# Kernel tuning notes

Hardware: AMD Instinct MI355X
Metric: run time of the kernel (lower is better)

## Reference

```python
import jax, jax.numpy as jnp
import numpy as np
import math

B, C, L = 16, 512, 1024
CONV_NUM, NUM_HEAD, K = 4, 8, 7
LN_EPS = 1e-5


def layer_norm(h, g, b):
    # h: [..., C], normalize over last dim (matches nn.LayerNorm(hidden_size))
    mean = jnp.mean(h, axis=-1, keepdims=True)
    var = jnp.mean(jnp.square(h - mean), axis=-1, keepdims=True)
    return (h - mean) / jnp.sqrt(var + LN_EPS) * g + b


def timing_signal(length, channels):
    nt = channels // 2
    pos = jnp.arange(length, dtype=jnp.float32)
    log_inc = math.log(10000.0) / (nt - 1)
    inv = jnp.exp(jnp.arange(nt, dtype=jnp.float32) * -log_inc)
    st = pos[:, None] * inv[None, :]
    sig = jnp.concatenate([jnp.sin(st), jnp.cos(st)], axis=1)  # [L, 2*nt]
    if channels % 2:
        sig = jnp.pad(sig, ((0, 0), (0, 1)))
    return sig  # [L, C]


def setup_inputs() -> dict:
    key = jax.random.key(0)
    ks = jax.random.split(key, 20)
    s = 0.02
    inp = {
        'x': jax.random.normal(ks[0], (B, C, L), jnp.float32),
        'mask': jax.random.randint(ks[1], (B, L), 0, 2, jnp.int32),
        'layer': 1,
        'num_blks': 7,
        'dw_w': jax.random.normal(ks[2], (CONV_NUM, C, 1, K), jnp.float32) * s,
        'pw_w': jax.random.normal(ks[3], (CONV_NUM, C, C), jnp.float32) * s,
        'pw_b': jnp.zeros((CONV_NUM, C), jnp.float32),
        'conv_ln_g': jnp.ones((CONV_NUM, C), jnp.float32),
        'conv_ln_b': jnp.zeros((CONV_NUM, C), jnp.float32),
        'w_kv': jax.random.normal(ks[4], (2 * C, C), jnp.float32) * s,
        'b_kv': jnp.zeros((2 * C,), jnp.float32),
        'w_q': jax.random.normal(ks[5], (C, C), jnp.float32) * s,
        'b_q': jnp.zeros((C,), jnp.float32),
        'ln_att_g': jnp.ones((C,), jnp.float32),
        'ln_att_b': jnp.zeros((C,), jnp.float32),
        'w_ffd1': jax.random.normal(ks[6], (C, C), jnp.float32) * s,
        'b_ffd1': jnp.zeros((C,), jnp.float32),
        'w_ffd2': jax.random.normal(ks[7], (C, C), jnp.float32) * s,
        'b_ffd2': jnp.zeros((C,), jnp.float32),
        'ln_ffd_g': jnp.ones((C,), jnp.float32),
        'ln_ffd_b': jnp.zeros((C,), jnp.float32),
    }
    return inp


def _forward(x, maskf, dw_w, pw_w, pw_b, conv_ln_g, conv_ln_b, w_kv, b_kv, w_q,
             b_q, ln_att_g, ln_att_b, w_ffd1, b_ffd1, w_ffd2, b_ffd2,
             ln_ffd_g, ln_ffd_b):
    # eval mode: dropout is identity and layer_dropout (stochastic depth) is
    # skipped entirely (the residual add only happens when self.training).
    b, c, l = x.shape
    out = x + timing_signal(l, c).T[None]  # [B,C,L]

    for i in range(CONV_NUM):
        h = layer_norm(out.transpose(0, 2, 1), conv_ln_g[i], conv_ln_b[i])
        h = h.transpose(0, 2, 1)  # [B,C,L]
        # depthwise conv, groups=C, padding=k//2, no bias
        h = jax.lax.conv_general_dilated(
            h, dw_w[i], window_strides=(1,), padding=[(K // 2, K // 2)],
            feature_group_count=c, dimension_numbers=('NCH', 'OIH', 'NCH'))
        # pointwise 1x1 conv + relu
        h = jnp.einsum('oc,bcl->bol', pw_w[i], h) + pw_b[i][None, :, None]
        out = jax.nn.relu(h)

    # self-attention sublayer
    h = layer_norm(out.transpose(0, 2, 1), ln_att_g, ln_att_b)  # [B,L,C]
    kv = jnp.einsum('oc,blc->blo', w_kv, h) + b_kv  # [B,L,2C]
    q = jnp.einsum('oc,blc->blo', w_q, h) + b_q     # [B,L,C]
    dh = c // NUM_HEAD
    Kh = kv[..., :c].reshape(b, l, NUM_HEAD, dh).transpose(0, 2, 1, 3)
    Vh = kv[..., c:].reshape(b, l, NUM_HEAD, dh).transpose(0, 2, 1, 3)
    Qh = q.reshape(b, l, NUM_HEAD, dh).transpose(0, 2, 1, 3) * (dh ** -0.5)
    logits = jnp.einsum('bhqd,bhkd->bhqk', Qh, Kh)  # [B,H,L,L]
    m = maskf[:, None, None, :]
    logits = logits * m + (1.0 - m) * -1e30
    w = jax.nn.softmax(logits, axis=-1)
    att = jnp.einsum('bhqk,bhkd->bhqd', w, Vh)
    out = att.transpose(0, 2, 1, 3).reshape(b, l, c).transpose(0, 2, 1)  # [B,C,L]

    # feed-forward sublayer (two 1x1 convs)
    h = layer_norm(out.transpose(0, 2, 1), ln_ffd_g, ln_ffd_b).transpose(0, 2, 1)
    h = jax.nn.relu(jnp.einsum('oc,bcl->bol', w_ffd1, h) + b_ffd1[None, :, None])
    out = jnp.einsum('oc,bcl->bol', w_ffd2, h) + b_ffd2[None, :, None]
    return out


def reference(x, mask, layer, num_blks, dw_w, pw_w, pw_b, conv_ln_g, conv_ln_b,
              w_kv, b_kv, w_q, b_q, ln_att_g, ln_att_b, w_ffd1, b_ffd1,
              w_ffd2, b_ffd2, ln_ffd_g, ln_ffd_b):
    del layer, num_blks  # only used by training-time stochastic depth
    return _forward(x, mask.astype(jnp.float32), dw_w, pw_w, pw_b, conv_ln_g,
                    conv_ln_b, w_kv, b_kv, w_q, b_q, ln_att_g, ln_att_b,
                    w_ffd1, b_ffd1, w_ffd2, b_ffd2, ln_ffd_g, ln_ffd_b)
```

## Files before the change

### kernel.cpp

```cpp
#include <hip/hip_runtime.h>
#include <math.h>

#define BB 16
#define CC 512
#define LL 1024
#define NHEAD 8
#define DH 64
#define KW 7

typedef unsigned short us;
typedef unsigned short us8 __attribute__((ext_vector_type(8)));
typedef unsigned short us4 __attribute__((ext_vector_type(4)));
typedef short mbf8 __attribute__((ext_vector_type(8)));
typedef float f32x4 __attribute__((ext_vector_type(4)));
typedef float f32x16 __attribute__((ext_vector_type(16)));

#define QSCALE 0.18033688f

__device__ inline us f2bf(float f) {
  union { float f; unsigned int u; } v; v.f = f;
  unsigned int u = v.u;
  u += 0x7fffu + ((u >> 16) & 1u);
  return (us)(u >> 16);
}
__device__ inline float bf2f(us s) {
  union { unsigned int u; float f; } v; v.u = ((unsigned int)s) << 16;
  return v.f;
}
__device__ __forceinline__ float fexp2(float x) {
  float r;
  asm("v_exp_f32 %0, %1" : "=v"(r) : "v"(x));
  return r;
}

__device__ __forceinline__ void gld16(const void* g, void* l) {
  __builtin_amdgcn_global_load_lds(
      (__attribute__((address_space(1))) unsigned int*)(uintptr_t)(g),
      (__attribute__((address_space(3))) unsigned int*)(unsigned int)(uintptr_t)(l),
      16, 0, 0);
}

__global__ __launch_bounds__(256) void k_cvtW(const float* __restrict__ pw,
                                              const float* __restrict__ wkv,
                                              const float* __restrict__ wq,
                                              const float* __restrict__ wf1,
                                              const float* __restrict__ wf2,
                                              us* __restrict__ dst) {
  int idx = blockIdx.x * 256 + threadIdx.x;
  int e = idx * 4;
  const int n2 = CC * CC;
  int r = e / n2, o = e - r * n2;
  const float* src; float sc = 1.0f;
  if (r < 4)       { src = pw + e; }
  else if (r == 4) { src = wkv + o; }
  else if (r == 5) { src = wq + o; sc = QSCALE; }
  else if (r == 6) { src = wkv + n2 + o; }
  else if (r == 7) { src = wf1 + o; }
  else             { src = wf2 + o; }
  float4 v = *(const float4*)src;
  us4 ov; ov[0] = f2bf(v.x * sc); ov[1] = f2bf(v.y * sc);
  ov[2] = f2bf(v.z * sc); ov[3] = f2bf(v.w * sc);
  *(us4*)(dst + e) = ov;
}

__global__ __launch_bounds__(256) void k_in_tr(const float* __restrict__ x,
                                               us* __restrict__ act) {
  __shared__ float xt[64][69];
  int t = threadIdx.x;
  int c0 = blockIdx.x * 64;
  int l0 = blockIdx.y * 64;
  int b  = blockIdx.z;
  {
    int r = t >> 2, lo2 = (t & 3) * 16;
    const float* src = x + ((size_t)b * CC + c0 + r) * LL + l0 + lo2;
#pragma unroll
    for (int q = 0; q < 4; ++q) {
      float4 v = *(const float4*)(src + q * 4);
      xt[r][lo2 + q * 4 + 0] = v.x; xt[r][lo2 + q * 4 + 1] = v.y;
      xt[r][lo2 + q * 4 + 2] = v.z; xt[r][lo2 + q * 4 + 3] = v.w;
    }
  }
  __syncthreads();
  const float log_inc = 9.210340371976184f / 255.0f;
  int lr = t >> 2, co = (t & 3) * 16;
  int l = l0 + lr;
  us obuf[16];
#pragma unroll
  for (int u = 0; u < 16; ++u) {
    int c = c0 + co + u;
    float inv = __expf(-(float)(c & 255) * log_inc);
    float st = (float)l * inv;
    float sg = (c < 256) ? sinf(st) : cosf(st);
    obuf[u] = f2bf(xt[co + u][lr] + sg);
  }
  us* dst = act + ((size_t)b * LL + l) * CC + c0 + co;
  *(us8*)dst = *(us8*)&obuf[0];
  *(us8*)(dst + 8) = *(us8*)&obuf[8];
}

__global__ __launch_bounds__(256) void k_ln(const us* __restrict__ in,
                                            const float* __restrict__ g,
                                            const float* __restrict__ bta,
                                            us* __restrict__ out) {
  int t = threadIdx.x;
  int lane = t & 63, w = t >> 6;
  size_t row = (size_t)blockIdx.x * 4 + w;
  const us* p = in + row * CC + lane * 8;
  us8 v = *(const us8*)p;
  float f[8]; float s = 0.f, ss = 0.f;
#pragma unroll
  for (int i = 0; i < 8; ++i) { f[i] = bf2f(v[i]); s += f[i]; ss += f[i] * f[i]; }
#pragma unroll
  for (int m = 1; m < 64; m <<= 1) { s += __shfl_xor(s, m); ss += __shfl_xor(ss, m); }
  float mean = s * (1.f / CC);
  float rstd = rsqrtf(ss * (1.f / CC) - mean * mean + 1e-5f);
  float4 g0 = *(const float4*)(g + lane * 8), g1 = *(const float4*)(g + lane * 8 + 4);
  float4 b0 = *(const float4*)(bta + lane * 8), b1 = *(const float4*)(bta + lane * 8 + 4);
  float gg[8] = {g0.x, g0.y, g0.z, g0.w, g1.x, g1.y, g1.z, g1.w};
  float bb2[8] = {b0.x, b0.y, b0.z, b0.w, b1.x, b1.y, b1.z, b1.w};
  us o[8];
#pragma unroll
  for (int i = 0; i < 8; ++i) o[i] = f2bf((f[i] - mean) * rstd * gg[i] + bb2[i]);
  *(us8*)(out + row * CC + lane * 8) = *(us8*)&o[0];
}

__global__ __launch_bounds__(256) void k_lndw(const us* __restrict__ in,
                                              const float* __restrict__ g,
                                              const float* __restrict__ bln,
                                              const float* __restrict__ w,
                                              us* __restrict__ out) {
  __shared__ float wld[KW * CC];
  __shared__ float stm[12], str[12];
  int t = threadIdx.x;
  int lane = t & 63, wv = t >> 6;
  for (int i = t; i < CC * KW; i += 256) {
    int j = i >> 9, c2 = i & (CC - 1);
    wld[i] = w[c2 * KW + j];
  }
  int rowid = blockIdx.x * 4;
  int l0 = rowid & (LL - 1);
  int b = rowid >> 10;
#pragma unroll
  for (int rr = 0; rr < 3; ++rr) {
    int slot = rr * 4 + wv;
    int r = l0 - 3 + slot;
    float mean = 0.f, rstd = 0.f;
    if (r >= 0 && r < LL) {
      us8 v = *(const us8*)(in + ((size_t)b * LL + r) * CC + lane * 8);
      float s = 0.f, ss = 0.f;
#pragma unroll
      for (int i = 0; i < 8; ++i) { float f = bf2f(v[i]); s += f; ss += f * f; }
#pragma unroll
      for (int m = 1; m < 64; m <<= 1) { s += __shfl_xor(s, m); ss += __shfl_xor(ss, m); }
      mean = s * (1.f / CC);
      rstd = rsqrtf(ss * (1.f / CC) - mean * mean + 1e-5f);
    }
    if (lane == 0) { stm[slot] = mean; str[slot] = rstd; }
  }
  __syncthreads();
  int c = lane * 8;
  int l = l0 + wv;
  float acc[8] = {}, ws[8] = {};
#pragma unroll
  for (int j = 0; j < KW; ++j) {
    int lj = l + j - 3;
    if (lj < 0 || lj >= LL) continue;
    int slot = lj - l0 + 3;
    float mean = stm[slot], rstd = str[slot];
    us8 v = *(const us8*)(in + ((size_t)b * LL + lj) * CC + c);
    float4 w0 = *(const float4*)&wld[j * CC + c];
    float4 w1 = *(const float4*)&wld[j * CC + c + 4];
    float wj[8] = {w0.x, w0.y, w0.z, w0.w, w1.x, w1.y, w1.z, w1.w};
#pragma unroll
    for (int u = 0; u < 8; ++u) {
      float nh = (bf2f(v[u]) - mean) * rstd;
      acc[u] += wj[u] * nh;
      ws[u] += wj[u];
    }
  }
  float4 g0 = *(const float4*)(g + c), g1 = *(const float4*)(g + c + 4);
  float4 b0 = *(const float4*)(bln + c), b1 = *(const float4*)(bln + c + 4);
  float gg[8] = {g0.x, g0.y, g0.z, g0.w, g1.x, g1.y, g1.z, g1.w};
  float bb2[8] = {b0.x, b0.y, b0.z, b0.w, b1.x, b1.y, b1.z, b1.w};
  us o[8];
#pragma unroll
  for (int u = 0; u < 8; ++u) o[u] = f2bf(gg[u] * acc[u] + bb2[u] * ws[u]);
  *(us8*)(out + ((size_t)b * LL + l) * CC + c) = *(us8*)&o[0];
}

template <int RELU, int F32OUT, int BIASMODE>
__global__ __launch_bounds__(256) void k_gemm(const us* __restrict__ A, long Ab,
                                              const us* __restrict__ Bm, long Bb,
                                              const float* __restrict__ bias,
                                              const float* __restrict__ bias2,
                                              void* __restrict__ outp,
                                              long orow, long obatch) {
  __shared__ __align__(16) us Ald[2][128 * 64];
  __shared__ __align__(16) us Bld[2][64 * 64];
  int t = threadIdx.x;
  int lane = t & 63, w = t >> 6;
  int wi = w >> 1, wj = w & 1;
  int gx = gridDim.x, gy = gridDim.y;
  int lin = blockIdx.x + gx * (blockIdx.y + gy * blockIdx.z);
  int nwg = gx * gy * gridDim.z;
  int swz = (lin & 7) * (nwg >> 3) + (lin >> 3);
  int bx = swz % gx; int rem = swz / gx; int by = rem % gy; int bz = rem / gy;
  int i0 = by * 128, j0 = bx * 64;
  const us* Ag = A + (size_t)bz * Ab + (size_t)i0 * 512;
  const us* Bg = Bm + (size_t)bz * Bb + (size_t)j0 * 512;
  int rr = lane >> 3, cc8 = (lane & 7) * 8;
  f32x4 acc[4][2];
  const f32x4 fz = {0.f, 0.f, 0.f, 0.f};
#pragma unroll
  for (int a = 0; a < 4; ++a)
#pragma unroll
    for (int c = 0; c < 2; ++c) acc[a][c] = fz;

#define STAGE(BUF, K0)                                                        \
  {                                                                           \
    _Pragma("unroll")                                                         \
    for (int it = 0; it < 4; ++it) {                                          \
      int ch = w * 4 + it;                                                    \
      gld16(Ag + (size_t)(ch * 8 + rr) * 512 + (K0) + cc8, &Ald[BUF][ch * 512]); \
    }                                                                         \
    _Pragma("unroll")                                                         \
    for (int it = 0; it < 2; ++it) {                                          \
      int ch = w * 2 + it;                                                    \
      gld16(Bg + (size_t)(ch * 8 + rr) * 512 + (K0) + cc8, &Bld[BUF][ch * 512]); \
    }                                                                         \
  }

  STAGE(0, 0)
#pragma unroll
  for (int tk = 0; tk < 8; ++tk) {
    int cur = tk & 1;
    __syncthreads();
    if (tk < 7) STAGE(cur ^ 1, (tk + 1) * 64)
    mbf8 af[4][2], bfr[2][2];
#pragma unroll
    for (int fi = 0; fi < 4; ++fi)
#pragma unroll
      for (int kh = 0; kh < 2; ++kh)
        af[fi][kh] = *(const mbf8*)&Ald[cur][(wi * 64 + fi * 16 + (lane & 15)) * 64 + kh * 32 + (lane >> 4) * 8];
#pragma unroll
    for (int fj = 0; fj < 2; ++fj)
#pragma unroll
      for (int kh = 0; kh < 2; ++kh)
        bfr[fj][kh] = *(const mbf8*)&Bld[cur][(wj * 32 + fj * 16 + (lane & 15)) * 64 + kh * 32 + (lane >> 4) * 8];
#pragma unroll
    for (int fi = 0; fi < 4; ++fi)
#pragma unroll
      for (int fj = 0; fj < 2; ++fj)
#pragma unroll
        for (int kh = 0; kh < 2; ++kh)
          acc[fi][fj] = __builtin_amdgcn_mfma_f32_16x16x32_bf16(af[fi][kh], bfr[fj][kh], acc[fi][fj], 0, 0, 0);
  }
#undef STAGE

#pragma unroll
  for (int fi = 0; fi < 4; ++fi)
#pragma unroll
    for (int fj = 0; fj < 2; ++fj) {
      int col = j0 + wj * 32 + fj * 16 + (lane & 15);
      float bv;
      if (BIASMODE == 2) bv = (col < CC) ? bias[col] : bias2[col - CC] * QSCALE;
      else if (BIASMODE == 0) bv = bias[col];
#pragma unroll
      for (int r = 0; r < 4; ++r) {
        int row = i0 + wi * 64 + fi * 16 + (lane >> 4) * 4 + r;
        float bvr = (BIASMODE == 1) ? bias[row] : bv;
        float v = acc[fi][fj][r] + bvr;
        if (RELU) v = fmaxf(v, 0.f);
        size_t off = (size_t)bz * obatch + (size_t)row * orow + col;
        if (F32OUT) ((float*)outp)[off] = v;
        else        ((us*)outp)[off] = f2bf(v);
      }
    }
}

__global__ __launch_bounds__(256) void k_attn(const us* __restrict__ KQ,
                                              const us* __restrict__ Vb,
                                              const int* __restrict__ mask,
                                              us* __restrict__ out) {
  __shared__ __align__(16) us Kld[64][72];
  __shared__ __align__(16) us Vld[64][72];
  __shared__ unsigned int mbits[32];
  int t = threadIdx.x;
  int lane = t & 63, w = t >> 6;
  int lo = lane & 31, hi = lane >> 5;
  int lin = blockIdx.x + 8 * (blockIdx.y + 8 * blockIdx.z);
  int swz = (lin & 7) * 128 + (lin >> 3);
  int q0 = (swz & 7) * 128;
  int h = (swz >> 3) & 7;
  int b = swz >> 6;

#pragma unroll
  for (int j = 0; j < 4; ++j) {
    int k = w * 256 + j * 64 + lane;
    unsigned long long bl = __ballot(mask[(size_t)b * LL + k] != 0);
    if (lane == 0) {
      mbits[w * 8 + j * 2]     = (unsigned int)bl;
      mbits[w * 8 + j * 2 + 1] = (unsigned int)(bl >> 32);
    }
  }

  mbf8 qf[4];
  {
    const us* qp = KQ + ((size_t)b * LL + q0 + w * 32 + lo) * 1024 + 512 + h * DH + hi * 8;
#pragma unroll
    for (int ds = 0; ds < 4; ++ds) qf[ds] = *(const mbf8*)(qp + ds * 16);
  }

  union { int i[4]; mbf8 v; } one;
  one.i[0] = 0x3F803F80; one.i[1] = 0x3F803F80; one.i[2] = 0x3F803F80; one.i[3] = 0x3F803F80;

  int sr = t >> 2, sko = (t & 3) * 16;
  const us* pkbase = KQ + ((size_t)b * LL + sr) * 1024 + h * DH + sko;
  const us* pvbase = Vb + ((size_t)b * CC + h * DH + sr) * LL + sko;
  us8 kr0 = *(const us8*)pkbase, kr1 = *(const us8*)(pkbase + 8);
  us8 vr0 = *(const us8*)pvbase, vr1 = *(const us8*)(pvbase + 8);

  const f32x16 Z16 = {0,0,0,0,0,0,0,0,0,0,0,0,0,0,0,0};
  f32x16 po0 = Z16, po1 = Z16, po2 = Z16;

  for (int kt = 0; kt < 16; ++kt) {
    asm volatile("s_waitcnt lgkmcnt(0)" ::: "memory");
    __builtin_amdgcn_s_barrier();
    asm volatile("" ::: "memory");
    *(us8*)&Kld[sr][sko]     = kr0;  *(us8*)&Kld[sr][sko + 8] = kr1;
    *(us8*)&Vld[sr][sko]     = vr0;  *(us8*)&Vld[sr][sko + 8] = vr1;
    if (kt < 15) {
      const us* pk = pkbase + (size_t)(kt + 1) * 64 * 1024;
      const us* pv = pvbase + (kt + 1) * 64;
      kr0 = *(const us8*)pk; kr1 = *(const us8*)(pk + 8);
      vr0 = *(const us8*)pv; vr1 = *(const us8*)(pv + 8);
    }
    asm volatile("s_waitcnt lgkmcnt(0)" ::: "memory");
    __builtin_amdgcn_s_barrier();
    asm volatile("" ::: "memory");

    uint2 mbp = *(const uint2*)&mbits[kt * 2];
    unsigned int b0 = (mbp.x >> lo) & 1u;
    unsigned int b1 = (mbp.y >> lo) & 1u;
    union { int i[4]; mbf8 v; } ma0, ma1;
    ma0.i[0] = (hi == 0 && !b0) ? 0xC348 : 0;
    ma0.i[1] = 0; ma0.i[2] = 0; ma0.i[3] = 0;
    ma1.i[0] = (hi == 0 && !b1) ? 0xC348 : 0;
    ma1.i[1] = 0; ma1.i[2] = 0; ma1.i[3] = 0;
    f32x16 s0 = __builtin_amdgcn_mfma_f32_32x32x16_bf16(ma0.v, one.v, Z16, 0, 0, 0);
    f32x16 s1 = __builtin_amdgcn_mfma_f32_32x32x16_bf16(ma1.v, one.v, Z16, 0, 0, 0);
#pragma unroll
    for (int ds = 0; ds < 4; ++ds) {
      mbf8 kf0 = *(const mbf8*)&Kld[lo][ds * 16 + hi * 8];
      mbf8 kf1 = *(const mbf8*)&Kld[32 + lo][ds * 16 + hi * 8];
      s0 = __builtin_amdgcn_mfma_f32_32x32x16_bf16(kf0, qf[ds], s0, 0, 0, 0);
      s1 = __builtin_amdgcn_mfma_f32_32x32x16_bf16(kf1, qf[ds], s1, 0, 0, 0);
    }
    float p0[16], p1[16];
#pragma unroll
    for (int r = 0; r < 16; ++r) { p0[r] = fexp2(s0[r]); p1[r] = fexp2(s1[r]); }

#define PVSTEP(P, KOFF, KS)                                                          \
    {                                                                                \
      int x0, x1, y0, y1;                                                            \
      asm("v_cvt_pk_bf16_f32 %0, %1, %2" : "=v"(x0) : "v"(P[8*KS+0]), "v"(P[8*KS+1])); \
      asm("v_cvt_pk_bf16_f32 %0, %1, %2" : "=v"(x1) : "v"(P[8*KS+2]), "v"(P[8*KS+3])); \
      asm("v_cvt_pk_bf16_f32 %0, %1, %2" : "=v"(y0) : "v"(P[8*KS+4]), "v"(P[8*KS+5])); \
      asm("v_cvt_pk_bf16_f32 %0, %1, %2" : "=v"(y1) : "v"(P[8*KS+6]), "v"(P[8*KS+7])); \
      asm("v_permlane32_swap_b32 %0, %1" : "+v"(x0), "+v"(y0));                      \
      asm("v_permlane32_swap_b32 %0, %1" : "+v"(x1), "+v"(y1));                      \
      union { int i[4]; mbf8 v; } fr;                                                \
      fr.i[0] = x0; fr.i[1] = x1; fr.i[2] = y0; fr.i[3] = y1;                        \
      mbf8 vf0 = *(const mbf8*)&Vld[lo][(KOFF) + (KS) * 16 + hi * 8];                \
      mbf8 vf1 = *(const mbf8*)&Vld[32 + lo][(KOFF) + (KS) * 16 + hi * 8];           \
      po0 = __builtin_amdgcn_mfma_f32_32x32x16_bf16(fr.v, vf0, po0, 0, 0, 0);        \
      po1 = __builtin_amdgcn_mfma_f32_32x32x16_bf16(fr.v, vf1, po1, 0, 0, 0);        \
      po2 = __builtin_amdgcn_mfma_f32_32x32x16_bf16(fr.v, one.v, po2, 0, 0, 0);      \
    }
    PVSTEP(p0, 0, 0)
    PVSTEP(p0, 0, 1)
    PVSTEP(p1, 32, 0)
    PVSTEP(p1, 32, 1)
#undef PVSTEP
  }

#define WRITEO(PO, DT)                                                               \
  {                                                                                  \
    _Pragma("unroll")                                                                \
    for (int r = 0; r < 16; ++r) {                                                   \
      int qrow = (r & 3) + 8 * (r >> 2) + 4 * hi;                                    \
      float iv = 1.0f / po2[r];                                                      \
      out[((size_t)b * LL + q0 + w * 32 + qrow) * CC + h * DH + (DT) * 32 + lo]      \
          = f2bf(PO[r] * iv);                                                        \
    }                                                                                \
  }
  WRITEO(po0, 0)
  WRITEO(po1, 1)
#undef WRITEO
}

extern "C" void kernel_launch(void* const* d_in, const int* in_sizes, int n_in,
                              void* d_out, int out_size, void* d_ws, size_t ws_size,
                              hipStream_t stream) {
  const float* x        = (const float*)d_in[0];
  const int*   mask     = (const int*)d_in[1];
  const float* dw_w     = (const float*)d_in[4];
  const float* pw_w     = (const float*)d_in[5];
  const float* pw_b     = (const float*)d_in[6];
  const float* cln_g    = (const float*)d_in[7];
  const float* cln_b    = (const float*)d_in[8];
  const float* w_kv     = (const float*)d_in[9];
  const float* b_kv     = (const float*)d_in[10];
  const float* w_q      = (const float*)d_in[11];
  const float* b_q      = (const float*)d_in[12];
  const float* ln_att_g = (const float*)d_in[13];
  const float* ln_att_b = (const float*)d_in[14];
  const float* w_ffd1   = (const float*)d_in[15];
  const float* b_ffd1   = (const float*)d_in[16];
  const float* w_ffd2   = (const float*)d_in[17];
  const float* b_ffd2   = (const float*)d_in[18];
  const float* ln_ffd_g = (const float*)d_in[19];
  const float* ln_ffd_b = (const float*)d_in[20];

  const size_t n2 = (size_t)CC * CC;
  size_t actElems = (size_t)BB * LL * CC;
  us* Wb = (us*)d_ws;
  us* pw_bf = Wb;
  us* kq_bf = Wb + 4 * n2;
  us* v_bf  = Wb + 6 * n2;
  us* f1_bf = Wb + 7 * n2;
  us* f2_bf = Wb + 8 * n2;
  us* A0 = Wb + 9 * n2;
  us* A1 = A0 + actElems;
  us* A2 = A1 + actElems;
  us* A3 = A2 + actElems;
  us* KQb = A1;

  long actB = (long)LL * CC;

  k_cvtW<<<2304, 256, 0, stream>>>(pw_w, w_kv, w_q, w_ffd1, w_ffd2, Wb);
  k_in_tr<<<dim3(8, 16, BB), 256, 0, stream>>>(x, A0);

  for (int i = 0; i < 4; ++i) {
    k_lndw<<<4096, 256, 0, stream>>>(A0, cln_g + i * CC, cln_b + i * CC,
                                     dw_w + (size_t)i * CC * KW, A3);
    k_gemm<1, 0, 0><<<dim3(8, 8, BB), 256, 0, stream>>>(
        A3, actB, pw_bf + (size_t)i * n2, 0, pw_b + i * CC, pw_b + i * CC,
        A0, 512, actB);
  }

  k_ln<<<4096, 256, 0, stream>>>(A0, ln_att_g, ln_att_b, A3);
  k_gemm<0, 0, 2><<<dim3(16, 8, BB), 256, 0, stream>>>(
      A3, actB, kq_bf, 0, b_kv, b_q, KQb, 1024, (long)LL * 1024);
  k_gemm<0, 0, 1><<<dim3(16, 4, BB), 256, 0, stream>>>(
      v_bf, 0, A3, actB, b_kv + CC, b_kv + CC, A0, 1024, actB);
  k_attn<<<dim3(8, NHEAD, BB), 256, 0, stream>>>(KQb, A0, mask, A3);

  k_ln<<<4096, 256, 0, stream>>>(A3, ln_ffd_g, ln_ffd_b, A0);
  k_gemm<1, 0, 0><<<dim3(8, 8, BB), 256, 0, stream>>>(
      A0, actB, f1_bf, 0, b_ffd1, b_ffd1, A1, 512, actB);
  k_gemm<0, 1, 1><<<dim3(16, 4, BB), 256, 0, stream>>>(
      f2_bf, 0, A1, actB, b_ffd2, b_ffd2, d_out, 1024, (long)CC * LL);
}
```

Baseline: 343.1 us.

## Load full B panel into swizzled LDS once, read A directly from global

```diff
diff --git a/kernel.cpp b/kernel.cpp
--- a/kernel.cpp
+++ b/kernel.cpp
@@ -195,8 +195,7 @@
                                               const float* __restrict__ bias2,
                                               void* __restrict__ outp,
                                               long orow, long obatch) {
-  __shared__ __align__(16) us Ald[2][128 * 64];
-  __shared__ __align__(16) us Bld[2][64 * 64];
+  __shared__ __align__(16) us Bld[64 * 512];
   int t = threadIdx.x;
   int lane = t & 63, w = t >> 6;
   int wi = w >> 1, wj = w & 1;
@@ -208,7 +207,15 @@
   int i0 = by * 128, j0 = bx * 64;
   const us* Ag = A + (size_t)bz * Ab + (size_t)i0 * 512;
   const us* Bg = Bm + (size_t)bz * Bb + (size_t)j0 * 512;
-  int rr = lane >> 3, cc8 = (lane & 7) * 8;
+
+#pragma unroll
+  for (int i = 0; i < 16; ++i) {
+    int r = w * 16 + i;
+    int sc = ((lane * 16) ^ ((r & 7) << 4)) >> 1;
+    gld16(Bg + (size_t)r * 512 + sc, &Bld[r * 512]);
+  }
+  __syncthreads();
+
   f32x4 acc[4][2];
   const f32x4 fz = {0.f, 0.f, 0.f, 0.f};
 #pragma unroll
@@ -216,37 +223,24 @@
 #pragma unroll
     for (int c = 0; c < 2; ++c) acc[a][c] = fz;
 
-#define STAGE(BUF, K0)                                                        \
-  {                                                                           \
-    _Pragma("unroll")                                                         \
-    for (int it = 0; it < 4; ++it) {                                          \
-      int ch = w * 4 + it;                                                    \
-      gld16(Ag + (size_t)(ch * 8 + rr) * 512 + (K0) + cc8, &Ald[BUF][ch * 512]); \
-    }                                                                         \
-    _Pragma("unroll")                                                         \
-    for (int it = 0; it < 2; ++it) {                                          \
-      int ch = w * 2 + it;                                                    \
-      gld16(Bg + (size_t)(ch * 8 + rr) * 512 + (K0) + cc8, &Bld[BUF][ch * 512]); \
-    }                                                                         \
-  }
-
-  STAGE(0, 0)
+  const us* Aw = Ag + (size_t)(wi * 64 + (lane & 15)) * 512 + (lane >> 4) * 8;
 #pragma unroll
   for (int tk = 0; tk < 8; ++tk) {
-    int cur = tk & 1;
-    __syncthreads();
-    if (tk < 7) STAGE(cur ^ 1, (tk + 1) * 64)
+    int k0 = tk * 64;
     mbf8 af[4][2], bfr[2][2];
 #pragma unroll
     for (int fi = 0; fi < 4; ++fi)
 #pragma unroll
       for (int kh = 0; kh < 2; ++kh)
-        af[fi][kh] = *(const mbf8*)&Ald[cur][(wi * 64 + fi * 16 + (lane & 15)) * 64 + kh * 32 + (lane >> 4) * 8];
+        af[fi][kh] = *(const mbf8*)(Aw + (size_t)(fi * 16) * 512 + k0 + kh * 32);
 #pragma unroll
     for (int fj = 0; fj < 2; ++fj)
 #pragma unroll
-      for (int kh = 0; kh < 2; ++kh)
-        bfr[fj][kh] = *(const mbf8*)&Bld[cur][(wj * 32 + fj * 16 + (lane & 15)) * 64 + kh * 32 + (lane >> 4) * 8];
+      for (int kh = 0; kh < 2; ++kh) {
+        int br = wj * 32 + fj * 16 + (lane & 15);
+        int cb = ((k0 + kh * 32 + (lane >> 4) * 8) * 2) ^ ((br & 7) << 4);
+        bfr[fj][kh] = *(const mbf8*)((const char*)&Bld[br * 512] + cb);
+      }
 #pragma unroll
     for (int fi = 0; fi < 4; ++fi)
 #pragma unroll
@@ -255,7 +249,6 @@
         for (int kh = 0; kh < 2; ++kh)
           acc[fi][fj] = __builtin_amdgcn_mfma_f32_16x16x32_bf16(af[fi][kh], bfr[fj][kh], acc[fi][fj], 0, 0, 0);
   }
-#undef STAGE
 
 #pragma unroll
   for (int fi = 0; fi < 4; ++fi)
```

Result: slower. 515.8 us (+50.3%).

## Process two 32-row query tiles per wave in attention kernel

Applied to the files above, without the earlier changes.

```diff
diff --git a/kernel.cpp b/kernel.cpp
--- a/kernel.cpp
+++ b/kernel.cpp
@@ -288,11 +288,11 @@
   int t = threadIdx.x;
   int lane = t & 63, w = t >> 6;
   int lo = lane & 31, hi = lane >> 5;
-  int lin = blockIdx.x + 8 * (blockIdx.y + 8 * blockIdx.z);
-  int swz = (lin & 7) * 128 + (lin >> 3);
-  int q0 = (swz & 7) * 128;
-  int h = (swz >> 3) & 7;
-  int b = swz >> 6;
+  int lin = blockIdx.x + 4 * (blockIdx.y + 8 * blockIdx.z);
+  int swz = (lin & 7) * 64 + (lin >> 3);
+  int q0 = (swz & 3) * 256;
+  int h = (swz >> 2) & 7;
+  int b = swz >> 5;
 
 #pragma unroll
   for (int j = 0; j < 4; ++j) {
@@ -304,11 +304,15 @@
     }
   }
 
-  mbf8 qf[4];
+  mbf8 qfA[4], qfB[4];
   {
-    const us* qp = KQ + ((size_t)b * LL + q0 + w * 32 + lo) * 1024 + 512 + h * DH + hi * 8;
-#pragma unroll
-    for (int ds = 0; ds < 4; ++ds) qf[ds] = *(const mbf8*)(qp + ds * 16);
+    const us* qpA = KQ + ((size_t)b * LL + q0 + w * 64 + lo) * 1024 + 512 + h * DH + hi * 8;
+    const us* qpB = qpA + (size_t)32 * 1024;
+#pragma unroll
+    for (int ds = 0; ds < 4; ++ds) {
+      qfA[ds] = *(const mbf8*)(qpA + ds * 16);
+      qfB[ds] = *(const mbf8*)(qpB + ds * 16);
+    }
   }
 
   union { int i[4]; mbf8 v; } one;
@@ -321,7 +325,7 @@
   us8 vr0 = *(const us8*)pvbase, vr1 = *(const us8*)(pvbase + 8);
 
   const f32x16 Z16 = {0,0,0,0,0,0,0,0,0,0,0,0,0,0,0,0};
-  f32x16 po0 = Z16, po1 = Z16, po2 = Z16;
+  f32x16 poA0 = Z16, poA1 = Z16, poB0 = Z16, poB1 = Z16, po2A = Z16, po2B = Z16;
 
   for (int kt = 0; kt < 16; ++kt) {
     asm volatile("s_waitcnt lgkmcnt(0)" ::: "memory");
@@ -347,20 +351,26 @@
     ma0.i[1] = 0; ma0.i[2] = 0; ma0.i[3] = 0;
     ma1.i[0] = (hi == 0 && !b1) ? 0xC348 : 0;
     ma1.i[1] = 0; ma1.i[2] = 0; ma1.i[3] = 0;
-    f32x16 s0 = __builtin_amdgcn_mfma_f32_32x32x16_bf16(ma0.v, one.v, Z16, 0, 0, 0);
-    f32x16 s1 = __builtin_amdgcn_mfma_f32_32x32x16_bf16(ma1.v, one.v, Z16, 0, 0, 0);
+    f32x16 sA0 = __builtin_amdgcn_mfma_f32_32x32x16_bf16(ma0.v, one.v, Z16, 0, 0, 0);
+    f32x16 sA1 = __builtin_amdgcn_mfma_f32_32x32x16_bf16(ma1.v, one.v, Z16, 0, 0, 0);
+    f32x16 sB0 = sA0, sB1 = sA1;
 #pragma unroll
     for (int ds = 0; ds < 4; ++ds) {
       mbf8 kf0 = *(const mbf8*)&Kld[lo][ds * 16 + hi * 8];
       mbf8 kf1 = *(const mbf8*)&Kld[32 + lo][ds * 16 + hi * 8];
-      s0 = __builtin_amdgcn_mfma_f32_32x32x16_bf16(kf0, qf[ds], s0, 0, 0, 0);
-      s1 = __builtin_amdgcn_mfma_f32_32x32x16_bf16(kf1, qf[ds], s1, 0, 0, 0);
-    }
-    float p0[16], p1[16];
-#pragma unroll
-    for (int r = 0; r < 16; ++r) { p0[r] = fexp2(s0[r]); p1[r] = fexp2(s1[r]); }
-
-#define PVSTEP(P, KOFF, KS)                                                          \
+      sA0 = __builtin_amdgcn_mfma_f32_32x32x16_bf16(kf0, qfA[ds], sA0, 0, 0, 0);
+      sA1 = __builtin_amdgcn_mfma_f32_32x32x16_bf16(kf1, qfA[ds], sA1, 0, 0, 0);
+      sB0 = __builtin_amdgcn_mfma_f32_32x32x16_bf16(kf0, qfB[ds], sB0, 0, 0, 0);
+      sB1 = __builtin_amdgcn_mfma_f32_32x32x16_bf16(kf1, qfB[ds], sB1, 0, 0, 0);
+    }
+    float pA0[16], pA1[16], pB0[16], pB1[16];
+#pragma unroll
+    for (int r = 0; r < 16; ++r) {
+      pA0[r] = fexp2(sA0[r]); pA1[r] = fexp2(sA1[r]);
+      pB0[r] = fexp2(sB0[r]); pB1[r] = fexp2(sB1[r]);
+    }
+
+#define CVT(P, KS, FR)                                                               \
     {                                                                                \
       int x0, x1, y0, y1;                                                            \
       asm("v_cvt_pk_bf16_f32 %0, %1, %2" : "=v"(x0) : "v"(P[8*KS+0]), "v"(P[8*KS+1])); \
@@ -369,33 +379,44 @@
       asm("v_cvt_pk_bf16_f32 %0, %1, %2" : "=v"(y1) : "v"(P[8*KS+6]), "v"(P[8*KS+7])); \
       asm("v_permlane32_swap_b32 %0, %1" : "+v"(x0), "+v"(y0));                      \
       asm("v_permlane32_swap_b32 %0, %1" : "+v"(x1), "+v"(y1));                      \
-      union { int i[4]; mbf8 v; } fr;                                                \
-      fr.i[0] = x0; fr.i[1] = x1; fr.i[2] = y0; fr.i[3] = y1;                        \
+      FR.i[0] = x0; FR.i[1] = x1; FR.i[2] = y0; FR.i[3] = y1;                        \
+    }
+#define PVSTEP(PA, PB, KOFF, KS)                                                     \
+    {                                                                                \
+      union { int i[4]; mbf8 v; } frA, frB;                                          \
+      CVT(PA, KS, frA)                                                               \
+      CVT(PB, KS, frB)                                                               \
       mbf8 vf0 = *(const mbf8*)&Vld[lo][(KOFF) + (KS) * 16 + hi * 8];                \
       mbf8 vf1 = *(const mbf8*)&Vld[32 + lo][(KOFF) + (KS) * 16 + hi * 8];           \
-      po0 = __builtin_amdgcn_mfma_f32_32x32x16_bf16(fr.v, vf0, po0, 0, 0, 0);        \
-      po1 = __builtin_amdgcn_mfma_f32_32x32x16_bf16(fr.v, vf1, po1, 0, 0, 0);        \
-      po2 = __builtin_amdgcn_mfma_f32_32x32x16_bf16(fr.v, one.v, po2, 0, 0, 0);      \
-    }
-    PVSTEP(p0, 0, 0)
-    PVSTEP(p0, 0, 1)
-    PVSTEP(p1, 32, 0)
-    PVSTEP(p1, 32, 1)
+      poA0 = __builtin_amdgcn_mfma_f32_32x32x16_bf16(frA.v, vf0, poA0, 0, 0, 0);     \
+      poA1 = __builtin_amdgcn_mfma_f32_32x32x16_bf16(frA.v, vf1, poA1, 0, 0, 0);     \
+      po2A = __builtin_amdgcn_mfma_f32_32x32x16_bf16(frA.v, one.v, po2A, 0, 0, 0);   \
+      poB0 = __builtin_amdgcn_mfma_f32_32x32x16_bf16(frB.v, vf0, poB0, 0, 0, 0);     \
+      poB1 = __builtin_amdgcn_mfma_f32_32x32x16_bf16(frB.v, vf1, poB1, 0, 0, 0);     \
+      po2B = __builtin_amdgcn_mfma_f32_32x32x16_bf16(frB.v, one.v, po2B, 0, 0, 0);   \
+    }
+    PVSTEP(pA0, pB0, 0, 0)
+    PVSTEP(pA0, pB0, 0, 1)
+    PVSTEP(pA1, pB1, 32, 0)
+    PVSTEP(pA1, pB1, 32, 1)
 #undef PVSTEP
-  }
-
-#define WRITEO(PO, DT)                                                               \
+#undef CVT
+  }
+
+#define WRITEO(PO, PO2, QOFF, DT)                                                    \
   {                                                                                  \
     _Pragma("unroll")                                                                \
     for (int r = 0; r < 16; ++r) {                                                   \
       int qrow = (r & 3) + 8 * (r >> 2) + 4 * hi;                                    \
-      float iv = 1.0f / po2[r];                                                      \
-      out[((size_t)b * LL + q0 + w * 32 + qrow) * CC + h * DH + (DT) * 32 + lo]      \
+      float iv = 1.0f / PO2[r];                                                      \
+      out[((size_t)b * LL + q0 + w * 64 + (QOFF) + qrow) * CC + h * DH + (DT) * 32 + lo] \
           = f2bf(PO[r] * iv);                                                        \
     }                                                                                \
   }
-  WRITEO(po0, 0)
-  WRITEO(po1, 1)
+  WRITEO(poA0, po2A, 0, 0)
+  WRITEO(poA1, po2A, 0, 1)
+  WRITEO(poB0, po2B, 32, 0)
+  WRITEO(poB1, po2B, 32, 1)
 #undef WRITEO
 }
 
@@ -454,7 +475,7 @@
       A3, actB, kq_bf, 0, b_kv, b_q, KQb, 1024, (long)LL * 1024);
   k_gemm<0, 0, 1><<<dim3(16, 4, BB), 256, 0, stream>>>(
       v_bf, 0, A3, actB, b_kv + CC, b_kv + CC, A0, 1024, actB);
-  k_attn<<<dim3(8, NHEAD, BB), 256, 0, stream>>>(KQb, A0, mask, A3);
+  k_attn<<<dim3(4, NHEAD, BB), 256, 0, stream>>>(KQb, A0, mask, A3);
 
   k_ln<<<4096, 256, 0, stream>>>(A3, ln_ffd_g, ln_ffd_b, A0);
   k_gemm<1, 0, 0><<<dim3(8, 8, BB), 256, 0, stream>>>(
```

After: 347.5 us. Within noise of the previous version (+1.3%).
